# Kernel optimization log

Hardware: AMD Instinct MI355X
Metric: run time of the kernel (lower is better)

## Reference

```python
import jax, jax.numpy as jnp
import numpy as np

N_NODES = 32768
N_EDGES = 65536
IN_DIM = 3      # node feature / edge attr dim (input_size)
HID = 64        # NNConv hidden/out channels
FC1 = 128


def setup_inputs() -> dict:
    key = jax.random.key(0)
    ks = jax.random.split(key, 16)
    inp = {}
    inp["x"] = jax.random.normal(ks[0], (N_NODES, IN_DIM), dtype=jnp.float32)
    inp["edge_index"] = jax.random.randint(ks[1], (2, N_EDGES), 0, N_NODES, dtype=jnp.int64)
    inp["edge_attr"] = jax.random.normal(ks[2], (N_EDGES, IN_DIM), dtype=jnp.float32)
    s = lambda fi, fo: 1.0 / np.sqrt(fi)
    # edge MLP 1: IN_DIM -> 64 -> IN_DIM*HID
    inp["W1a"] = jax.random.normal(ks[3], (IN_DIM, 64), dtype=jnp.float32) * s(IN_DIM, 64)
    inp["b1a"] = jnp.zeros((64,), dtype=jnp.float32)
    inp["W1b"] = jax.random.normal(ks[4], (64, IN_DIM * HID), dtype=jnp.float32) * s(64, IN_DIM * HID)
    inp["b1b"] = jnp.zeros((IN_DIM * HID,), dtype=jnp.float32)
    inp["root1"] = jax.random.normal(ks[5], (IN_DIM, HID), dtype=jnp.float32) * s(IN_DIM, HID)
    inp["bias1"] = jnp.zeros((HID,), dtype=jnp.float32)
    # edge MLP 2: IN_DIM -> 64 -> HID*HID
    inp["W2a"] = jax.random.normal(ks[6], (IN_DIM, 64), dtype=jnp.float32) * s(IN_DIM, 64)
    inp["b2a"] = jnp.zeros((64,), dtype=jnp.float32)
    inp["W2b"] = jax.random.normal(ks[7], (64, HID * HID), dtype=jnp.float32) * s(64, HID * HID)
    inp["b2b"] = jnp.zeros((HID * HID,), dtype=jnp.float32)
    inp["root2"] = jax.random.normal(ks[8], (HID, HID), dtype=jnp.float32) * s(HID, HID)
    inp["bias2"] = jnp.zeros((HID,), dtype=jnp.float32)
    # fc1
    inp["Wf"] = jax.random.normal(ks[9], (HID, FC1), dtype=jnp.float32) * s(HID, FC1)
    inp["bf"] = jnp.zeros((FC1,), dtype=jnp.float32)
    return inp


def _nnconv(x, src, dst, edge_attr, Wa, ba, Wb, bb, root, bias, in_c, out_c):
    # per-edge weight matrix from edge MLP: [E, in_c, out_c]
    h = jax.nn.relu(edge_attr @ Wa + ba)
    W_e = (h @ Wb + bb).reshape(-1, in_c, out_c)
    # gather source features, transform per edge: [E, out_c]
    msg = jnp.einsum('ei,eio->eo', x[src], W_e)
    # scatter-mean into target nodes
    summed = jax.ops.segment_sum(msg, dst, num_segments=N_NODES)
    cnt = jax.ops.segment_sum(jnp.ones((msg.shape[0],), msg.dtype), dst, num_segments=N_NODES)
    agg = summed / jnp.maximum(cnt, 1.0)[:, None]
    return agg + x @ root + bias


def reference(x, edge_index, edge_attr, W1a, b1a, W1b, b1b, root1, bias1,
              W2a, b2a, W2b, b2b, root2, bias2, Wf, bf):
    src, dst = edge_index[0], edge_index[1]
    h = jax.nn.elu(_nnconv(x, src, dst, edge_attr, W1a, b1a, W1b, b1b, root1, bias1, IN_DIM, HID))
    h = jax.nn.elu(_nnconv(h, src, dst, edge_attr, W2a, b2a, W2b, b2b, root2, bias2, HID, HID))
    h = jax.nn.elu(h @ Wf + bf)
    # dropout is identity in eval mode
    return h
```

## Files before the change

### kernel.cpp

```cpp
#include <hip/hip_runtime.h>
#include <math.h>

#define NN 32768
#define NE 65536

typedef __attribute__((ext_vector_type(8))) short bf16x8;
typedef __attribute__((ext_vector_type(4))) float f32x4;

__device__ __forceinline__ float elu_f(float v) {
    return v > 0.f ? v : (expf(v) - 1.f);
}
__device__ __forceinline__ unsigned short bf16_rn(float f) {
    unsigned u = __float_as_uint(f);
    return (unsigned short)((u + 0x7FFFu + ((u >> 16) & 1u)) >> 16);
}
__device__ __forceinline__ float bf16_to_f(unsigned short h) {
    return __uint_as_float(((unsigned)h) << 16);
}

#define FMA8(Cj, aj, b0, b1) \
    Cj[0] += (aj)*(b0).x; Cj[1] += (aj)*(b0).y; Cj[2] += (aj)*(b0).z; Cj[3] += (aj)*(b0).w; \
    Cj[4] += (aj)*(b1).x; Cj[5] += (aj)*(b1).y; Cj[6] += (aj)*(b1).z; Cj[7] += (aj)*(b1).w;

__global__ void k_hist(const int* __restrict__ ei, int* __restrict__ cnt) {
    int e = blockIdx.x * 256 + threadIdx.x;
    if (e < NE) atomicAdd(&cnt[ei[NE + e]], 1);
}

__global__ __launch_bounds__(1024) void k_scan(const int* __restrict__ cnt,
                                               int* __restrict__ start,
                                               int* __restrict__ cursor) {
    __shared__ int wtot[16];
    const int t = threadIdx.x;
    const int lane = t & 63, wave = t >> 6;
    int local[32];
    const int base = t * 32;
    int s = 0;
    #pragma unroll
    for (int j = 0; j < 32; ++j) { local[j] = s; s += cnt[base + j]; }
    const int tot = s;
    int sc = tot;
    #pragma unroll
    for (int off = 1; off < 64; off <<= 1) {
        int v = __shfl_up(sc, off, 64);
        if (lane >= off) sc += v;
    }
    if (lane == 63) wtot[wave] = sc;
    __syncthreads();
    if (t == 0) {
        int run = 0;
        #pragma unroll
        for (int w = 0; w < 16; ++w) { int v = wtot[w]; wtot[w] = run; run += v; }
    }
    __syncthreads();
    const int tbase = wtot[wave] + (sc - tot);
    #pragma unroll
    for (int j = 0; j < 32; ++j) {
        int v = tbase + local[j];
        start[base + j] = v;
        cursor[base + j] = v;
    }
}

__global__ void k_fill(const int* __restrict__ ei, int* __restrict__ cursor,
                       int* __restrict__ perm) {
    int e = blockIdx.x * 256 + threadIdx.x;
    if (e < NE) {
        int d = ei[NE + e];
        int pos = atomicAdd(&cursor[d], 1);
        perm[pos] = e;
    }
}

__global__ void k_prep(const float* __restrict__ W2b, short* __restrict__ BT) {
    int idx = blockIdx.x * 256 + threadIdx.x;
    int col = idx >> 6;
    int k   = idx & 63;
    float f = W2b[(size_t)k * 4096 + col];
    unsigned short hi = bf16_rn(f);
    unsigned short lo = bf16_rn(f - bf16_to_f(hi));
    int i = col >> 6, o = col & 63;
    size_t base = (size_t)i * 9216;
    BT[base + o * 72 + k]        = (short)hi;
    BT[base + 4608 + o * 72 + k] = (short)lo;
}

__global__ __launch_bounds__(256, 2) void k1_conv1(
    const float* __restrict__ x, const int* __restrict__ ei,
    const float* __restrict__ eatt, const int* __restrict__ perm,
    const float* __restrict__ W1a, const float* __restrict__ b1a,
    const float* __restrict__ W1b, const float* __restrict__ b1b,
    float* __restrict__ msg1)
{
    __shared__ float sW1b[64 * 192];
    __shared__ float sb1b[192];
    __shared__ float sW1a[192];
    __shared__ float sb1a[64];
    __shared__ float sxs[256 * 4];
    __shared__ float sea[256 * 4];
    const int tid = threadIdx.x;
    const int e0 = blockIdx.x * 256;

    for (int u = tid; u < 64 * 192 / 4; u += 256)
        ((float4*)sW1b)[u] = ((const float4*)W1b)[u];
    if (tid < 192) { sW1a[tid] = W1a[tid]; sb1b[tid] = b1b[tid]; }
    if (tid < 64)  sb1a[tid] = b1a[tid];
    {
        int pe = perm[e0 + tid];
        int s = ei[pe];
        sxs[tid*4+0] = x[s*3+0];
        sxs[tid*4+1] = x[s*3+1];
        sxs[tid*4+2] = x[s*3+2];
        sea[tid*4+0] = eatt[pe*3+0];
        sea[tid*4+1] = eatt[pe*3+1];
        sea[tid*4+2] = eatt[pe*3+2];
    }
    __syncthreads();

    const int ty = tid >> 3;
    const int tx = tid & 7;
    const int eb = ty * 8;
    const int o0 = tx * 8;

    float xs_r[8][3], ea_r[8][3];
    #pragma unroll
    for (int j = 0; j < 8; ++j)
        #pragma unroll
        for (int i = 0; i < 3; ++i) {
            xs_r[j][i] = sxs[(eb + j) * 4 + i];
            ea_r[j][i] = sea[(eb + j) * 4 + i];
        }

    float C[8][8];
    #pragma unroll
    for (int j = 0; j < 8; ++j)
        #pragma unroll
        for (int l = 0; l < 8; ++l) C[j][l] = 0.f;

    for (int k = 0; k < 64; ++k) {
        float hh[8];
        #pragma unroll
        for (int j = 0; j < 8; ++j) {
            float h = sb1a[k] + ea_r[j][0]*sW1a[k] + ea_r[j][1]*sW1a[64+k] + ea_r[j][2]*sW1a[128+k];
            hh[j] = fmaxf(h, 0.f);
        }
        #pragma unroll
        for (int i = 0; i < 3; ++i) {
            const float4* wp = (const float4*)&sW1b[k*192 + i*64 + o0];
            float4 w0 = wp[0], w1 = wp[1];
            float a[8];
            #pragma unroll
            for (int j = 0; j < 8; ++j) a[j] = hh[j] * xs_r[j][i];
            #pragma unroll
            for (int j = 0; j < 8; ++j) { FMA8(C[j], a[j], w0, w1); }
        }
    }
    #pragma unroll
    for (int i = 0; i < 3; ++i) {
        const float4* wp = (const float4*)&sb1b[i*64 + o0];
        float4 w0 = wp[0], w1 = wp[1];
        #pragma unroll
        for (int j = 0; j < 8; ++j) {
            float a = xs_r[j][i];
            FMA8(C[j], a, w0, w1);
        }
    }
    #pragma unroll
    for (int j = 0; j < 8; ++j) {
        float* p = msg1 + (size_t)(e0 + eb + j) * 64 + o0;
        float4 v0 = { C[j][0], C[j][1], C[j][2], C[j][3] };
        float4 v1 = { C[j][4], C[j][5], C[j][6], C[j][7] };
        *(float4*)p       = v0;
        *(float4*)(p + 4) = v1;
    }
}

__global__ __launch_bounds__(256) void k2_node1(
    const float* __restrict__ msg1, const int* __restrict__ start,
    const int* __restrict__ cnt,
    const float* __restrict__ x, const float* __restrict__ root1,
    const float* __restrict__ bias1, float* __restrict__ h1)
{
    __shared__ float sR[192], sb[64];
    const int tid = threadIdx.x;
    if (tid < 192) sR[tid] = root1[tid];
    if (tid < 64)  sb[tid] = bias1[tid];
    __syncthreads();
    const int n = blockIdx.x * 64 + (tid >> 2);
    const int c = (tid & 3) * 16;
    const int st = start[n], num = cnt[n];
    float acc[16];
    #pragma unroll
    for (int l = 0; l < 16; ++l) acc[l] = 0.f;
    for (int d = 0; d < num; ++d) {
        const float* row = &msg1[(size_t)(st + d) * 64 + c];
        #pragma unroll
        for (int q = 0; q < 4; ++q) {
            float4 v = *(const float4*)(row + q * 4);
            acc[q*4+0] += v.x; acc[q*4+1] += v.y; acc[q*4+2] += v.z; acc[q*4+3] += v.w;
        }
    }
    const float inv = 1.f / fmaxf((float)num, 1.f);
    const float x0 = x[n*3+0], x1 = x[n*3+1], x2 = x[n*3+2];
    float* hp = &h1[(size_t)n * 64 + c];
    #pragma unroll
    for (int q = 0; q < 4; ++q) {
        float4 ov;
        float* o4 = (float*)&ov;
        #pragma unroll
        for (int l = 0; l < 4; ++l) {
            int o = c + q*4 + l;
            float v = acc[q*4+l] * inv + sb[o] + x0*sR[o] + x1*sR[64+o] + x2*sR[128+o];
            o4[l] = elu_f(v);
        }
        *(float4*)(hp + q*4) = ov;
    }
}

__global__ __launch_bounds__(256, 1) void k3_mfma(
    const float* __restrict__ h1, const int* __restrict__ ei,
    const float* __restrict__ eatt, const int* __restrict__ perm,
    const float* __restrict__ W2a, const float* __restrict__ b2a,
    const short* __restrict__ BT, const float* __restrict__ b2b,
    float* __restrict__ msg2)
{
    __shared__ __align__(16) float sX[17408];
    __shared__ __align__(16) short sB[2][9216];
    __shared__ float sbb[4096];
    __shared__ float sw2a[192];
    __shared__ float sb2a2[64];

    const int tid = threadIdx.x;
    const int e0  = blockIdx.x * 256;
    const int wid = tid >> 6;
    const int lane = tid & 63;
    const int l15 = lane & 15, lhi = lane >> 4;

    if (tid < 192) sw2a[tid] = W2a[tid];
    if (tid < 64)  sb2a2[tid] = b2a[tid];
    for (int u = tid; u < 1024; u += 256) ((float4*)sbb)[u] = ((const float4*)b2b)[u];
    const int pe = perm[e0 + tid];
    const int esrc = ei[pe];
    float ea0 = eatt[pe*3+0], ea1 = eatt[pe*3+1], ea2 = eatt[pe*3+2];
    __syncthreads();

    for (int k = 0; k < 64; ++k) {
        float h = sb2a2[k] + ea0*sw2a[k] + ea1*sw2a[64+k] + ea2*sw2a[128+k];
        sX[tid*68 + k] = fmaxf(h, 0.f);
    }
    __syncthreads();

    bf16x8 ah[4][2], al[4][2];
    #pragma unroll
    for (int rt = 0; rt < 4; ++rt)
        #pragma unroll
        for (int kc = 0; kc < 2; ++kc) {
            const float* p = &sX[(wid*64 + rt*16 + l15)*68 + kc*32 + lhi*8];
            bf16x8 H, L;
            #pragma unroll
            for (int j = 0; j < 8; ++j) {
                float f = p[j];
                unsigned short hh = bf16_rn(f);
                unsigned short ll = bf16_rn(f - bf16_to_f(hh));
                H[j] = (short)hh; L[j] = (short)ll;
            }
            ah[rt][kc] = H; al[rt][kc] = L;
        }
    __syncthreads();

    {
        const float* row = h1 + (size_t)esrc * 64;
        #pragma unroll
        for (int it = 0; it < 16; ++it) {
            float4 vv = *(const float4*)(row + it*4);
            sX[(it*4+0)*260 + tid] = vv.x;
            sX[(it*4+1)*260 + tid] = vv.y;
            sX[(it*4+2)*260 + tid] = vv.z;
            sX[(it*4+3)*260 + tid] = vv.w;
        }
    }
    {
        const unsigned* src = (const unsigned*)BT;
        unsigned* dst = (unsigned*)sB[0];
        #pragma unroll
        for (int j = 0; j < 18; ++j) dst[tid + 256*j] = src[tid + 256*j];
    }
    __syncthreads();

    f32x4 acc[4][4];
    #pragma unroll
    for (int rt = 0; rt < 4; ++rt)
        #pragma unroll
        for (int ot = 0; ot < 4; ++ot) { acc[rt][ot][0]=0.f; acc[rt][ot][1]=0.f; acc[rt][ot][2]=0.f; acc[rt][ot][3]=0.f; }

    int cur = 0;
    for (int i = 0; i < 64; ++i) {
        unsigned pf[18];
        if (i < 63) {
            const unsigned* src = (const unsigned*)(BT + (size_t)(i+1) * 9216);
            #pragma unroll
            for (int j = 0; j < 18; ++j) pf[j] = src[tid + 256*j];
        }
        float vv[4][4];
        #pragma unroll
        for (int rt = 0; rt < 4; ++rt) {
            f32x4 t4 = *(const f32x4*)&sX[i*260 + wid*64 + rt*16 + lhi*4];
            vv[rt][0]=t4[0]; vv[rt][1]=t4[1]; vv[rt][2]=t4[2]; vv[rt][3]=t4[3];
        }
        const short* Bh = &sB[cur][0];
        const short* Bl = &sB[cur][4608];
        #pragma unroll
        for (int ot = 0; ot < 4; ++ot) {
            const int ob = (ot*16 + l15)*72 + lhi*8;
            bf16x8 bh0 = *(const bf16x8*)&Bh[ob];
            bf16x8 bh1 = *(const bf16x8*)&Bh[ob + 32];
            bf16x8 bl0 = *(const bf16x8*)&Bl[ob];
            bf16x8 bl1 = *(const bf16x8*)&Bl[ob + 32];
            float bb = sbb[i*64 + ot*16 + l15];
            #pragma unroll
            for (int rt = 0; rt < 4; ++rt) {
                f32x4 t = {0.f, 0.f, 0.f, 0.f};
                t = __builtin_amdgcn_mfma_f32_16x16x32_bf16(ah[rt][0], bh0, t, 0, 0, 0);
                t = __builtin_amdgcn_mfma_f32_16x16x32_bf16(al[rt][0], bh0, t, 0, 0, 0);
                t = __builtin_amdgcn_mfma_f32_16x16x32_bf16(ah[rt][0], bl0, t, 0, 0, 0);
                t = __builtin_amdgcn_mfma_f32_16x16x32_bf16(ah[rt][1], bh1, t, 0, 0, 0);
                t = __builtin_amdgcn_mfma_f32_16x16x32_bf16(al[rt][1], bh1, t, 0, 0, 0);
                t = __builtin_amdgcn_mfma_f32_16x16x32_bf16(ah[rt][1], bl1, t, 0, 0, 0);
                #pragma unroll
                for (int r = 0; r < 4; ++r)
                    acc[rt][ot][r] += vv[rt][r] * (t[r] + bb);
            }
        }
        if (i < 63) {
            unsigned* dst = (unsigned*)sB[cur ^ 1];
            #pragma unroll
            for (int j = 0; j < 18; ++j) dst[tid + 256*j] = pf[j];
            cur ^= 1;
        }
        __syncthreads();
    }

    #pragma unroll
    for (int rt = 0; rt < 4; ++rt) {
        const int rowb = e0 + wid*64 + rt*16 + lhi*4;
        #pragma unroll
        for (int ot = 0; ot < 4; ++ot) {
            const int o = ot*16 + l15;
            #pragma unroll
            for (int r = 0; r < 4; ++r)
                msg2[(size_t)(rowb + r)*64 + o] = acc[rt][ot][r];
        }
    }
}

__global__ __launch_bounds__(256, 2) void k4_final(
    const float* __restrict__ msg2, const int* __restrict__ start,
    const int* __restrict__ cnt,
    const float* __restrict__ h1,
    const float* __restrict__ root2, const float* __restrict__ bias2,
    const float* __restrict__ Wf, const float* __restrict__ bf,
    float* __restrict__ out)
{
    __shared__ float sh1[32 * 65];
    __shared__ float sh2[32 * 65];
    __shared__ float sR[64 * 64];
    __shared__ float sW[64 * 128];
    __shared__ float sb2[64];
    __shared__ float sbf[128];
    __shared__ float sinv[32];
    __shared__ int   sstart[32];
    __shared__ int   scnt[32];
    const int tid = threadIdx.x;
    const int n0 = blockIdx.x * 32;

    for (int u = tid; u < 64*64/4; u += 256) ((float4*)sR)[u] = ((const float4*)root2)[u];
    for (int u = tid; u < 64*128/4; u += 256) ((float4*)sW)[u] = ((const float4*)Wf)[u];
    if (tid < 64)  sb2[tid] = bias2[tid];
    if (tid < 128) sbf[tid] = bf[tid];
    if (tid < 32) {
        int n = n0 + tid;
        int cc = cnt[n];
        sstart[tid] = start[n];
        scnt[tid] = cc;
        sinv[tid] = 1.f / fmaxf((float)cc, 1.f);
    }
    for (int u = tid; u < 32 * 16; u += 256) {
        int n = u >> 4, i4 = (u & 15) * 4;
        float4 v = *(const float4*)&h1[(size_t)(n0 + n) * 64 + i4];
        sh1[n*65+i4] = v.x; sh1[n*65+i4+1] = v.y; sh1[n*65+i4+2] = v.z; sh1[n*65+i4+3] = v.w;
    }
    __syncthreads();

    {
        const int tn = tid >> 4;
        const int o0 = (tid & 15) * 4;
        float acc[2][4];
        #pragma unroll
        for (int j = 0; j < 2; ++j) {
            int ln = tn * 2 + j;
            int st = sstart[ln], num = scnt[ln];
            float4 a = {0.f, 0.f, 0.f, 0.f};
            for (int d = 0; d < num; ++d) {
                float4 s = *(const float4*)&msg2[(size_t)(st + d) * 64 + o0];
                a.x += s.x; a.y += s.y; a.z += s.z; a.w += s.w;
            }
            float inv = sinv[ln];
            acc[j][0] = a.x*inv + sb2[o0+0];
            acc[j][1] = a.y*inv + sb2[o0+1];
            acc[j][2] = a.z*inv + sb2[o0+2];
            acc[j][3] = a.w*inv + sb2[o0+3];
        }
        #pragma unroll 8
        for (int k = 0; k < 64; ++k) {
            float4 r = *(const float4*)&sR[k*64 + o0];
            float h0 = sh1[(tn*2)*65 + k];
            float h1v = sh1[(tn*2+1)*65 + k];
            acc[0][0] += h0*r.x; acc[0][1] += h0*r.y; acc[0][2] += h0*r.z; acc[0][3] += h0*r.w;
            acc[1][0] += h1v*r.x; acc[1][1] += h1v*r.y; acc[1][2] += h1v*r.z; acc[1][3] += h1v*r.w;
        }
        #pragma unroll
        for (int j = 0; j < 2; ++j) {
            int n = tn * 2 + j;
            #pragma unroll
            for (int l = 0; l < 4; ++l) sh2[n*65 + o0 + l] = elu_f(acc[j][l]);
        }
    }
    __syncthreads();

    {
        const int tn = tid >> 4;
        const int c0 = (tid & 15) * 8;
        float acc[2][8];
        #pragma unroll
        for (int j = 0; j < 2; ++j)
            #pragma unroll
            for (int l = 0; l < 8; ++l) acc[j][l] = sbf[c0 + l];
        #pragma unroll 8
        for (int k = 0; k < 64; ++k) {
            float4 w0 = *(const float4*)&sW[k*128 + c0];
            float4 w1 = *(const float4*)&sW[k*128 + c0 + 4];
            float h0 = sh2[(tn*2)*65 + k];
            float h1v = sh2[(tn*2+1)*65 + k];
            FMA8(acc[0], h0, w0, w1);
            FMA8(acc[1], h1v, w0, w1);
        }
        #pragma unroll
        for (int j = 0; j < 2; ++j) {
            size_t n = n0 + tn * 2 + j;
            float4 oA, oB;
            oA.x = elu_f(acc[j][0]); oA.y = elu_f(acc[j][1]); oA.z = elu_f(acc[j][2]); oA.w = elu_f(acc[j][3]);
            oB.x = elu_f(acc[j][4]); oB.y = elu_f(acc[j][5]); oB.z = elu_f(acc[j][6]); oB.w = elu_f(acc[j][7]);
            *(float4*)&out[n*128 + c0]     = oA;
            *(float4*)&out[n*128 + c0 + 4] = oB;
        }
    }
}

extern "C" void kernel_launch(void* const* d_in, const int* in_sizes, int n_in,
                              void* d_out, int out_size, void* d_ws, size_t ws_size,
                              hipStream_t stream)
{
    const float* x     = (const float*)d_in[0];
    const int*   ei    = (const int*)d_in[1];
    const float* ea    = (const float*)d_in[2];
    const float* W1a   = (const float*)d_in[3];
    const float* b1a   = (const float*)d_in[4];
    const float* W1b   = (const float*)d_in[5];
    const float* b1b   = (const float*)d_in[6];
    const float* root1 = (const float*)d_in[7];
    const float* bias1 = (const float*)d_in[8];
    const float* W2a   = (const float*)d_in[9];
    const float* b2a   = (const float*)d_in[10];
    const float* W2b   = (const float*)d_in[11];
    const float* b2b   = (const float*)d_in[12];
    const float* root2 = (const float*)d_in[13];
    const float* bias2 = (const float*)d_in[14];
    const float* Wf    = (const float*)d_in[15];
    const float* bf    = (const float*)d_in[16];
    float* out = (float*)d_out;

    float* ws    = (float*)d_ws;
    float* msg1  = ws;
    float* msg2  = ws + 4194304;
    float* h1    = ws + 8388608;
    short* BT    = (short*)(ws + 10485760);
    int*   cnt_i = (int*)(ws + 10780672);
    int*   startp= (int*)(ws + 10813440);
    int*   cursor= (int*)(ws + 10846208);
    int*   perm  = (int*)(ws + 10878976);

    hipMemsetAsync(cnt_i, 0, (size_t)NN * sizeof(int), stream);

    k_prep  <<<1024,      256, 0, stream>>>(W2b, BT);
    k_hist  <<<NE/256,    256, 0, stream>>>(ei, cnt_i);
    k_scan  <<<1,        1024, 0, stream>>>(cnt_i, startp, cursor);
    k_fill  <<<NE/256,    256, 0, stream>>>(ei, cursor, perm);
    k1_conv1<<<NE/256,    256, 0, stream>>>(x, ei, ea, perm, W1a, b1a, W1b, b1b, msg1);
    k2_node1<<<NN/64,     256, 0, stream>>>(msg1, startp, cnt_i, x, root1, bias1, h1);
    k3_mfma <<<NE/256,    256, 0, stream>>>(h1, ei, ea, perm, W2a, b2a, BT, b2b, msg2);
    k4_final<<<NN/32,     256, 0, stream>>>(msg2, startp, cnt_i, h1, root2, bias2, Wf, bf, out);
}
```

Before: 291.0 us.

## Restructure edge convs: MFMA conv1, swap k3 operand roles, gather via perm

Conv1's per-edge message is now computed with split-bf16 MFMA from a pre-packed W1b. Conv2's MFMA is reorganised: the gathered source features become the A operand and the loop runs over the 64 hidden units, with the edge-MLP activation applied as a scalar. The bias is handled as a 65th step. Edges are processed in original order (128 per block, two blocks per CU) and the node-side reductions index messages through perm. Weight tiles are streamed into LDS with global_load_lds double buffering, and the prep and histogram kernels are merged into one launch. The risk is scattered perm-indexed reads in the reduction kernels and the extra MFMA iteration.

```diff
diff --git a/kernel.cpp b/kernel.cpp
--- a/kernel.cpp
+++ b/kernel.cpp
@@ -17,14 +17,49 @@
 __device__ __forceinline__ float bf16_to_f(unsigned short h) {
     return __uint_as_float(((unsigned)h) << 16);
 }
+__device__ __forceinline__ void gld16(const void* g, void* l) {
+    __builtin_amdgcn_global_load_lds(
+        (const __attribute__((address_space(1))) unsigned int*)g,
+        (__attribute__((address_space(3))) unsigned int*)l, 16, 0, 0);
+}
 
 #define FMA8(Cj, aj, b0, b1) \
     Cj[0] += (aj)*(b0).x; Cj[1] += (aj)*(b0).y; Cj[2] += (aj)*(b0).z; Cj[3] += (aj)*(b0).w; \
     Cj[4] += (aj)*(b1).x; Cj[5] += (aj)*(b1).y; Cj[6] += (aj)*(b1).z; Cj[7] += (aj)*(b1).w;
 
-__global__ void k_hist(const int* __restrict__ ei, int* __restrict__ cnt) {
-    int e = blockIdx.x * 256 + threadIdx.x;
-    if (e < NE) atomicAdd(&cnt[ei[NE + e]], 1);
+__global__ void k_prep2(const float* __restrict__ W2b, const float* __restrict__ b2b,
+                        const float* __restrict__ W1b, const int* __restrict__ ei,
+                        short* __restrict__ BT2, short* __restrict__ BT1,
+                        int* __restrict__ cnt) {
+    int g = blockIdx.x * 256 + threadIdx.x;
+    if (g < 262144) {
+        float f = W2b[g];
+        int o = g & 63, i = (g >> 6) & 63, k = g >> 12;
+        unsigned short hi = bf16_rn(f);
+        unsigned short lo = bf16_rn(f - bf16_to_f(hi));
+        BT2[(size_t)k * 9216 + o * 72 + i]        = (short)hi;
+        BT2[(size_t)k * 9216 + 4608 + o * 72 + i] = (short)lo;
+    } else if (g < 266240) {
+        int g2 = g - 262144;
+        float f = b2b[g2];
+        int o = g2 & 63, i = g2 >> 6;
+        unsigned short hi = bf16_rn(f);
+        unsigned short lo = bf16_rn(f - bf16_to_f(hi));
+        BT2[(size_t)64 * 9216 + o * 72 + i]        = (short)hi;
+        BT2[(size_t)64 * 9216 + 4608 + o * 72 + i] = (short)lo;
+    } else if (g < 278528) {
+        int g2 = g - 266240;
+        float f = W1b[g2];
+        int col = g2 % 192, k = g2 / 192;
+        int c = col >> 6, o = col & 63;
+        unsigned short hi = bf16_rn(f);
+        unsigned short lo = bf16_rn(f - bf16_to_f(hi));
+        BT1[c * 9216 + o * 72 + k]        = (short)hi;
+        BT1[c * 9216 + 4608 + o * 72 + k] = (short)lo;
+    } else {
+        int e = g - 278528;
+        atomicAdd(&cnt[ei[NE + e]], 1);
+    }
 }
 
 __global__ __launch_bounds__(1024) void k_scan(const int* __restrict__ cnt,
@@ -72,243 +107,87 @@
     }
 }
 
-__global__ void k_prep(const float* __restrict__ W2b, short* __restrict__ BT) {
-    int idx = blockIdx.x * 256 + threadIdx.x;
-    int col = idx >> 6;
-    int k   = idx & 63;
-    float f = W2b[(size_t)k * 4096 + col];
-    unsigned short hi = bf16_rn(f);
-    unsigned short lo = bf16_rn(f - bf16_to_f(hi));
-    int i = col >> 6, o = col & 63;
-    size_t base = (size_t)i * 9216;
-    BT[base + o * 72 + k]        = (short)hi;
-    BT[base + 4608 + o * 72 + k] = (short)lo;
-}
-
 __global__ __launch_bounds__(256, 2) void k1_conv1(
     const float* __restrict__ x, const int* __restrict__ ei,
-    const float* __restrict__ eatt, const int* __restrict__ perm,
+    const float* __restrict__ eatt,
     const float* __restrict__ W1a, const float* __restrict__ b1a,
-    const float* __restrict__ W1b, const float* __restrict__ b1b,
+    const short* __restrict__ BT1, const float* __restrict__ b1b,
     float* __restrict__ msg1)
 {
-    __shared__ float sW1b[64 * 192];
-    __shared__ float sb1b[192];
+    __shared__ __align__(16) short sBT1[3 * 9216];
+    __shared__ float sxs[128 * 4];
+    __shared__ float sea[128 * 4];
     __shared__ float sW1a[192];
     __shared__ float sb1a[64];
-    __shared__ float sxs[256 * 4];
-    __shared__ float sea[256 * 4];
+    __shared__ float sb1b[192];
+
     const int tid = threadIdx.x;
-    const int e0 = blockIdx.x * 256;
-
-    for (int u = tid; u < 64 * 192 / 4; u += 256)
-        ((float4*)sW1b)[u] = ((const float4*)W1b)[u];
+    const int e0  = blockIdx.x * 128;
+    const int wid = tid >> 6;
+    const int lane = tid & 63;
+    const int l15 = lane & 15, lhi = lane >> 4;
+
+    {
+        const char* src = (const char*)BT1;
+        char* dst = (char*)&sBT1[0];
+        for (int j = wid; j < 54; j += 4)
+            gld16(src + j * 1024 + lane * 16, dst + j * 1024);
+    }
     if (tid < 192) { sW1a[tid] = W1a[tid]; sb1b[tid] = b1b[tid]; }
     if (tid < 64)  sb1a[tid] = b1a[tid];
-    {
-        int pe = perm[e0 + tid];
-        int s = ei[pe];
+    if (tid < 128) {
+        int e = e0 + tid;
+        int s = ei[e];
         sxs[tid*4+0] = x[s*3+0];
         sxs[tid*4+1] = x[s*3+1];
         sxs[tid*4+2] = x[s*3+2];
-        sea[tid*4+0] = eatt[pe*3+0];
-        sea[tid*4+1] = eatt[pe*3+1];
-        sea[tid*4+2] = eatt[pe*3+2];
-    }
-    __syncthreads();
-
-    const int ty = tid >> 3;
-    const int tx = tid & 7;
-    const int eb = ty * 8;
-    const int o0 = tx * 8;
-
-    float xs_r[8][3], ea_r[8][3];
-    #pragma unroll
-    for (int j = 0; j < 8; ++j)
-        #pragma unroll
-        for (int i = 0; i < 3; ++i) {
-            xs_r[j][i] = sxs[(eb + j) * 4 + i];
-            ea_r[j][i] = sea[(eb + j) * 4 + i];
-        }
-
-    float C[8][8];
-    #pragma unroll
-    for (int j = 0; j < 8; ++j)
-        #pragma unroll
-        for (int l = 0; l < 8; ++l) C[j][l] = 0.f;
-
-    for (int k = 0; k < 64; ++k) {
-        float hh[8];
-        #pragma unroll
-        for (int j = 0; j < 8; ++j) {
-            float h = sb1a[k] + ea_r[j][0]*sW1a[k] + ea_r[j][1]*sW1a[64+k] + ea_r[j][2]*sW1a[128+k];
-            hh[j] = fmaxf(h, 0.f);
-        }
-        #pragma unroll
-        for (int i = 0; i < 3; ++i) {
-            const float4* wp = (const float4*)&sW1b[k*192 + i*64 + o0];
-            float4 w0 = wp[0], w1 = wp[1];
-            float a[8];
-            #pragma unroll
-            for (int j = 0; j < 8; ++j) a[j] = hh[j] * xs_r[j][i];
-            #pragma unroll
-            for (int j = 0; j < 8; ++j) { FMA8(C[j], a[j], w0, w1); }
-        }
-    }
-    #pragma unroll
-    for (int i = 0; i < 3; ++i) {
-        const float4* wp = (const float4*)&sb1b[i*64 + o0];
-        float4 w0 = wp[0], w1 = wp[1];
-        #pragma unroll
-        for (int j = 0; j < 8; ++j) {
-            float a = xs_r[j][i];
-            FMA8(C[j], a, w0, w1);
-        }
-    }
-    #pragma unroll
-    for (int j = 0; j < 8; ++j) {
-        float* p = msg1 + (size_t)(e0 + eb + j) * 64 + o0;
-        float4 v0 = { C[j][0], C[j][1], C[j][2], C[j][3] };
-        float4 v1 = { C[j][4], C[j][5], C[j][6], C[j][7] };
-        *(float4*)p       = v0;
-        *(float4*)(p + 4) = v1;
-    }
-}
-
-__global__ __launch_bounds__(256) void k2_node1(
-    const float* __restrict__ msg1, const int* __restrict__ start,
-    const int* __restrict__ cnt,
-    const float* __restrict__ x, const float* __restrict__ root1,
-    const float* __restrict__ bias1, float* __restrict__ h1)
-{
-    __shared__ float sR[192], sb[64];
-    const int tid = threadIdx.x;
-    if (tid < 192) sR[tid] = root1[tid];
-    if (tid < 64)  sb[tid] = bias1[tid];
-    __syncthreads();
-    const int n = blockIdx.x * 64 + (tid >> 2);
-    const int c = (tid & 3) * 16;
-    const int st = start[n], num = cnt[n];
-    float acc[16];
-    #pragma unroll
-    for (int l = 0; l < 16; ++l) acc[l] = 0.f;
-    for (int d = 0; d < num; ++d) {
-        const float* row = &msg1[(size_t)(st + d) * 64 + c];
-        #pragma unroll
-        for (int q = 0; q < 4; ++q) {
-            float4 v = *(const float4*)(row + q * 4);
-            acc[q*4+0] += v.x; acc[q*4+1] += v.y; acc[q*4+2] += v.z; acc[q*4+3] += v.w;
-        }
-    }
-    const float inv = 1.f / fmaxf((float)num, 1.f);
-    const float x0 = x[n*3+0], x1 = x[n*3+1], x2 = x[n*3+2];
-    float* hp = &h1[(size_t)n * 64 + c];
-    #pragma unroll
-    for (int q = 0; q < 4; ++q) {
-        float4 ov;
-        float* o4 = (float*)&ov;
-        #pragma unroll
-        for (int l = 0; l < 4; ++l) {
-            int o = c + q*4 + l;
-            float v = acc[q*4+l] * inv + sb[o] + x0*sR[o] + x1*sR[64+o] + x2*sR[128+o];
-            o4[l] = elu_f(v);
-        }
-        *(float4*)(hp + q*4) = ov;
-    }
-}
-
-__global__ __launch_bounds__(256, 1) void k3_mfma(
-    const float* __restrict__ h1, const int* __restrict__ ei,
-    const float* __restrict__ eatt, const int* __restrict__ perm,
-    const float* __restrict__ W2a, const float* __restrict__ b2a,
-    const short* __restrict__ BT, const float* __restrict__ b2b,
-    float* __restrict__ msg2)
-{
-    __shared__ __align__(16) float sX[17408];
-    __shared__ __align__(16) short sB[2][9216];
-    __shared__ float sbb[4096];
-    __shared__ float sw2a[192];
-    __shared__ float sb2a2[64];
-
-    const int tid = threadIdx.x;
-    const int e0  = blockIdx.x * 256;
-    const int wid = tid >> 6;
-    const int lane = tid & 63;
-    const int l15 = lane & 15, lhi = lane >> 4;
-
-    if (tid < 192) sw2a[tid] = W2a[tid];
-    if (tid < 64)  sb2a2[tid] = b2a[tid];
-    for (int u = tid; u < 1024; u += 256) ((float4*)sbb)[u] = ((const float4*)b2b)[u];
-    const int pe = perm[e0 + tid];
-    const int esrc = ei[pe];
-    float ea0 = eatt[pe*3+0], ea1 = eatt[pe*3+1], ea2 = eatt[pe*3+2];
-    __syncthreads();
-
-    for (int k = 0; k < 64; ++k) {
-        float h = sb2a2[k] + ea0*sw2a[k] + ea1*sw2a[64+k] + ea2*sw2a[128+k];
-        sX[tid*68 + k] = fmaxf(h, 0.f);
-    }
-    __syncthreads();
-
-    bf16x8 ah[4][2], al[4][2];
-    #pragma unroll
-    for (int rt = 0; rt < 4; ++rt)
+        sea[tid*4+0] = eatt[e*3+0];
+        sea[tid*4+1] = eatt[e*3+1];
+        sea[tid*4+2] = eatt[e*3+2];
+    }
+    __syncthreads();
+
+    bf16x8 ah[2][2], al[2][2];
+    #pragma unroll
+    for (int rt = 0; rt < 2; ++rt) {
+        const int arow = wid*32 + rt*16 + l15;
+        const float a0 = sea[arow*4+0], a1 = sea[arow*4+1], a2 = sea[arow*4+2];
         #pragma unroll
         for (int kc = 0; kc < 2; ++kc) {
-            const float* p = &sX[(wid*64 + rt*16 + l15)*68 + kc*32 + lhi*8];
+            const int kb = kc*32 + lhi*8;
             bf16x8 H, L;
             #pragma unroll
             for (int j = 0; j < 8; ++j) {
-                float f = p[j];
+                int k = kb + j;
+                float f = fmaxf(sb1a[k] + a0*sW1a[k] + a1*sW1a[64+k] + a2*sW1a[128+k], 0.f);
                 unsigned short hh = bf16_rn(f);
                 unsigned short ll = bf16_rn(f - bf16_to_f(hh));
                 H[j] = (short)hh; L[j] = (short)ll;
             }
             ah[rt][kc] = H; al[rt][kc] = L;
         }
-    __syncthreads();
-
-    {
-        const float* row = h1 + (size_t)esrc * 64;
-        #pragma unroll
-        for (int it = 0; it < 16; ++it) {
-            float4 vv = *(const float4*)(row + it*4);
-            sX[(it*4+0)*260 + tid] = vv.x;
-            sX[(it*4+1)*260 + tid] = vv.y;
-            sX[(it*4+2)*260 + tid] = vv.z;
-            sX[(it*4+3)*260 + tid] = vv.w;
-        }
-    }
-    {
-        const unsigned* src = (const unsigned*)BT;
-        unsigned* dst = (unsigned*)sB[0];
-        #pragma unroll
-        for (int j = 0; j < 18; ++j) dst[tid + 256*j] = src[tid + 256*j];
-    }
-    __syncthreads();
-
-    f32x4 acc[4][4];
-    #pragma unroll
-    for (int rt = 0; rt < 4; ++rt)
+    }
+    float xr[2][4][3];
+    #pragma unroll
+    for (int rt = 0; rt < 2; ++rt)
+        #pragma unroll
+        for (int r = 0; r < 4; ++r) {
+            int crow = wid*32 + rt*16 + lhi*4 + r;
+            xr[rt][r][0] = sxs[crow*4+0];
+            xr[rt][r][1] = sxs[crow*4+1];
+            xr[rt][r][2] = sxs[crow*4+2];
+        }
+
+    f32x4 acc[2][4];
+    #pragma unroll
+    for (int rt = 0; rt < 2; ++rt)
         #pragma unroll
         for (int ot = 0; ot < 4; ++ot) { acc[rt][ot][0]=0.f; acc[rt][ot][1]=0.f; acc[rt][ot][2]=0.f; acc[rt][ot][3]=0.f; }
 
-    int cur = 0;
-    for (int i = 0; i < 64; ++i) {
-        unsigned pf[18];
-        if (i < 63) {
-            const unsigned* src = (const unsigned*)(BT + (size_t)(i+1) * 9216);
-            #pragma unroll
-            for (int j = 0; j < 18; ++j) pf[j] = src[tid + 256*j];
-        }
-        float vv[4][4];
-        #pragma unroll
-        for (int rt = 0; rt < 4; ++rt) {
-            f32x4 t4 = *(const f32x4*)&sX[i*260 + wid*64 + rt*16 + lhi*4];
-            vv[rt][0]=t4[0]; vv[rt][1]=t4[1]; vv[rt][2]=t4[2]; vv[rt][3]=t4[3];
-        }
-        const short* Bh = &sB[cur][0];
-        const short* Bl = &sB[cur][4608];
+    #pragma unroll
+    for (int c = 0; c < 3; ++c) {
+        const short* Bh = &sBT1[c * 9216];
+        const short* Bl = Bh + 4608;
         #pragma unroll
         for (int ot = 0; ot < 4; ++ot) {
             const int ob = (ot*16 + l15)*72 + lhi*8;
@@ -316,9 +195,8 @@
             bf16x8 bh1 = *(const bf16x8*)&Bh[ob + 32];
             bf16x8 bl0 = *(const bf16x8*)&Bl[ob];
             bf16x8 bl1 = *(const bf16x8*)&Bl[ob + 32];
-            float bb = sbb[i*64 + ot*16 + l15];
-            #pragma unroll
-            for (int rt = 0; rt < 4; ++rt) {
+            #pragma unroll
+            for (int rt = 0; rt < 2; ++rt) {
                 f32x4 t = {0.f, 0.f, 0.f, 0.f};
                 t = __builtin_amdgcn_mfma_f32_16x16x32_bf16(ah[rt][0], bh0, t, 0, 0, 0);
                 t = __builtin_amdgcn_mfma_f32_16x16x32_bf16(al[rt][0], bh0, t, 0, 0, 0);
@@ -328,34 +206,211 @@
                 t = __builtin_amdgcn_mfma_f32_16x16x32_bf16(ah[rt][1], bl1, t, 0, 0, 0);
                 #pragma unroll
                 for (int r = 0; r < 4; ++r)
-                    acc[rt][ot][r] += vv[rt][r] * (t[r] + bb);
-            }
-        }
-        if (i < 63) {
-            unsigned* dst = (unsigned*)sB[cur ^ 1];
-            #pragma unroll
-            for (int j = 0; j < 18; ++j) dst[tid + 256*j] = pf[j];
-            cur ^= 1;
-        }
-        __syncthreads();
-    }
-
-    #pragma unroll
-    for (int rt = 0; rt < 4; ++rt) {
-        const int rowb = e0 + wid*64 + rt*16 + lhi*4;
+                    acc[rt][ot][r] += xr[rt][r][c] * t[r];
+            }
+        }
+    }
+    #pragma unroll
+    for (int rt = 0; rt < 2; ++rt) {
         #pragma unroll
         for (int ot = 0; ot < 4; ++ot) {
             const int o = ot*16 + l15;
-            #pragma unroll
-            for (int r = 0; r < 4; ++r)
-                msg2[(size_t)(rowb + r)*64 + o] = acc[rt][ot][r];
-        }
-    }
+            const float b0 = sb1b[o], b1 = sb1b[64+o], b2 = sb1b[128+o];
+            #pragma unroll
+            for (int r = 0; r < 4; ++r) {
+                float v = acc[rt][ot][r] + xr[rt][r][0]*b0 + xr[rt][r][1]*b1 + xr[rt][r][2]*b2;
+                int row = e0 + wid*32 + rt*16 + lhi*4 + r;
+                msg1[(size_t)row * 64 + o] = v;
+            }
+        }
+    }
+}
+
+__global__ __launch_bounds__(256) void k2_node1(
+    const float* __restrict__ msg1, const int* __restrict__ start,
+    const int* __restrict__ cnt, const int* __restrict__ perm,
+    const float* __restrict__ x, const float* __restrict__ root1,
+    const float* __restrict__ bias1, float* __restrict__ h1)
+{
+    __shared__ float sR[192], sb[64];
+    const int tid = threadIdx.x;
+    if (tid < 192) sR[tid] = root1[tid];
+    if (tid < 64)  sb[tid] = bias1[tid];
+    __syncthreads();
+    const int n = blockIdx.x * 64 + (tid >> 2);
+    const int c = (tid & 3) * 16;
+    const int st = start[n], num = cnt[n];
+    float acc[16];
+    #pragma unroll
+    for (int l = 0; l < 16; ++l) acc[l] = 0.f;
+    for (int d = 0; d < num; ++d) {
+        const int row = perm[st + d];
+        const float* rp = &msg1[(size_t)row * 64 + c];
+        #pragma unroll
+        for (int q = 0; q < 4; ++q) {
+            float4 v = *(const float4*)(rp + q * 4);
+            acc[q*4+0] += v.x; acc[q*4+1] += v.y; acc[q*4+2] += v.z; acc[q*4+3] += v.w;
+        }
+    }
+    const float inv = 1.f / fmaxf((float)num, 1.f);
+    const float x0 = x[n*3+0], x1 = x[n*3+1], x2 = x[n*3+2];
+    float* hp = &h1[(size_t)n * 64 + c];
+    #pragma unroll
+    for (int q = 0; q < 4; ++q) {
+        float4 ov;
+        float* o4 = (float*)&ov;
+        #pragma unroll
+        for (int l = 0; l < 4; ++l) {
+            int o = c + q*4 + l;
+            float v = acc[q*4+l] * inv + sb[o] + x0*sR[o] + x1*sR[64+o] + x2*sR[128+o];
+            o4[l] = elu_f(v);
+        }
+        *(float4*)(hp + q*4) = ov;
+    }
+}
+
+__global__ __launch_bounds__(256, 2) void k3_mfma(
+    const float* __restrict__ h1, const int* __restrict__ ei,
+    const float* __restrict__ eatt,
+    const float* __restrict__ W2a, const float* __restrict__ b2a,
+    const short* __restrict__ BT2,
+    float* __restrict__ msg2)
+{
+    __shared__ __align__(16) float sV[128 * 68];
+    __shared__ __align__(16) short sB[2][9216];
+    __shared__ float sea[128 * 4];
+    __shared__ float sW2a[192];
+    __shared__ float sb2a[64];
+
+    const int tid = threadIdx.x;
+    const int e0  = blockIdx.x * 128;
+    const int wid = tid >> 6;
+    const int lane = tid & 63;
+    const int l15 = lane & 15, lhi = lane >> 4;
+
+    {
+        const char* src = (const char*)BT2;
+        char* dst = (char*)&sB[0][0];
+        for (int j = wid; j < 18; j += 4)
+            gld16(src + j * 1024 + lane * 16, dst + j * 1024);
+    }
+    if (tid < 192) sW2a[tid] = W2a[tid];
+    if (tid < 64)  sb2a[tid] = b2a[tid];
+    if (tid < 128) {
+        int e = e0 + tid;
+        sea[tid*4+0] = eatt[e*3+0];
+        sea[tid*4+1] = eatt[e*3+1];
+        sea[tid*4+2] = eatt[e*3+2];
+    }
+    {
+        const int edge = tid >> 1, half = tid & 1;
+        const int s = ei[e0 + edge];
+        const float* row = h1 + (size_t)s * 64 + half * 32;
+        float* dst = &sV[edge * 68 + half * 32];
+        #pragma unroll
+        for (int q = 0; q < 8; ++q)
+            *(float4*)(dst + q*4) = *(const float4*)(row + q*4);
+    }
+    __syncthreads();
+
+    bf16x8 vh[2][2], vl[2][2];
+    #pragma unroll
+    for (int rt = 0; rt < 2; ++rt)
+        #pragma unroll
+        for (int kc = 0; kc < 2; ++kc) {
+            const float* p = &sV[(wid*32 + rt*16 + l15)*68 + kc*32 + lhi*8];
+            bf16x8 H, L;
+            #pragma unroll
+            for (int j = 0; j < 8; ++j) {
+                float f = p[j];
+                unsigned short hh = bf16_rn(f);
+                unsigned short ll = bf16_rn(f - bf16_to_f(hh));
+                H[j] = (short)hh; L[j] = (short)ll;
+            }
+            vh[rt][kc] = H; vl[rt][kc] = L;
+        }
+    float er[2][4][3];
+    #pragma unroll
+    for (int rt = 0; rt < 2; ++rt)
+        #pragma unroll
+        for (int r = 0; r < 4; ++r) {
+            int row = wid*32 + rt*16 + lhi*4 + r;
+            er[rt][r][0] = sea[row*4+0];
+            er[rt][r][1] = sea[row*4+1];
+            er[rt][r][2] = sea[row*4+2];
+        }
+
+    f32x4 acc[2][4];
+    #pragma unroll
+    for (int rt = 0; rt < 2; ++rt)
+        #pragma unroll
+        for (int ot = 0; ot < 4; ++ot) { acc[rt][ot][0]=0.f; acc[rt][ot][1]=0.f; acc[rt][ot][2]=0.f; acc[rt][ot][3]=0.f; }
+
+    int cur = 0;
+    for (int k = 0; k <= 64; ++k) {
+        if (k < 64) {
+            const char* src = (const char*)(BT2 + (size_t)(k + 1) * 9216);
+            char* dst = (char*)&sB[cur ^ 1][0];
+            for (int j = wid; j < 18; j += 4)
+                gld16(src + j * 1024 + lane * 16, dst + j * 1024);
+        }
+        float us[2][4];
+        if (k < 64) {
+            const float wa = sW2a[k], wb = sW2a[64+k], wc = sW2a[128+k], bb = sb2a[k];
+            #pragma unroll
+            for (int rt = 0; rt < 2; ++rt)
+                #pragma unroll
+                for (int r = 0; r < 4; ++r)
+                    us[rt][r] = fmaxf(bb + er[rt][r][0]*wa + er[rt][r][1]*wb + er[rt][r][2]*wc, 0.f);
+        } else {
+            #pragma unroll
+            for (int rt = 0; rt < 2; ++rt)
+                #pragma unroll
+                for (int r = 0; r < 4; ++r) us[rt][r] = 1.f;
+        }
+        const short* Bh = &sB[cur][0];
+        const short* Bl = &sB[cur][4608];
+        #pragma unroll
+        for (int ot = 0; ot < 4; ++ot) {
+            const int ob = (ot*16 + l15)*72 + lhi*8;
+            bf16x8 bh0 = *(const bf16x8*)&Bh[ob];
+            bf16x8 bh1 = *(const bf16x8*)&Bh[ob + 32];
+            bf16x8 bl0 = *(const bf16x8*)&Bl[ob];
+            bf16x8 bl1 = *(const bf16x8*)&Bl[ob + 32];
+            #pragma unroll
+            for (int rt = 0; rt < 2; ++rt) {
+                f32x4 t = {0.f, 0.f, 0.f, 0.f};
+                t = __builtin_amdgcn_mfma_f32_16x16x32_bf16(vh[rt][0], bh0, t, 0, 0, 0);
+                t = __builtin_amdgcn_mfma_f32_16x16x32_bf16(vl[rt][0], bh0, t, 0, 0, 0);
+                t = __builtin_amdgcn_mfma_f32_16x16x32_bf16(vh[rt][0], bl0, t, 0, 0, 0);
+                t = __builtin_amdgcn_mfma_f32_16x16x32_bf16(vh[rt][1], bh1, t, 0, 0, 0);
+                t = __builtin_amdgcn_mfma_f32_16x16x32_bf16(vl[rt][1], bh1, t, 0, 0, 0);
+                t = __builtin_amdgcn_mfma_f32_16x16x32_bf16(vh[rt][1], bl1, t, 0, 0, 0);
+                #pragma unroll
+                for (int r = 0; r < 4; ++r)
+                    acc[rt][ot][r] += us[rt][r] * t[r];
+            }
+        }
+        __syncthreads();
+        if (k < 64) cur ^= 1;
+    }
+
+    #pragma unroll
+    for (int rt = 0; rt < 2; ++rt)
+        #pragma unroll
+        for (int ot = 0; ot < 4; ++ot) {
+            const int o = ot*16 + l15;
+            #pragma unroll
+            for (int r = 0; r < 4; ++r) {
+                int row = e0 + wid*32 + rt*16 + lhi*4 + r;
+                msg2[(size_t)row * 64 + o] = acc[rt][ot][r];
+            }
+        }
 }
 
 __global__ __launch_bounds__(256, 2) void k4_final(
     const float* __restrict__ msg2, const int* __restrict__ start,
-    const int* __restrict__ cnt,
+    const int* __restrict__ cnt, const int* __restrict__ perm,
     const float* __restrict__ h1,
     const float* __restrict__ root2, const float* __restrict__ bias2,
     const float* __restrict__ Wf, const float* __restrict__ bf,
@@ -401,7 +456,8 @@
             int st = sstart[ln], num = scnt[ln];
             float4 a = {0.f, 0.f, 0.f, 0.f};
             for (int d = 0; d < num; ++d) {
-                float4 s = *(const float4*)&msg2[(size_t)(st + d) * 64 + o0];
+                int row = perm[st + d];
+                float4 s = *(const float4*)&msg2[(size_t)row * 64 + o0];
                 a.x += s.x; a.y += s.y; a.z += s.z; a.w += s.w;
             }
             float inv = sinv[ln];
@@ -483,20 +539,20 @@
     float* msg1  = ws;
     float* msg2  = ws + 4194304;
     float* h1    = ws + 8388608;
-    short* BT    = (short*)(ws + 10485760);
-    int*   cnt_i = (int*)(ws + 10780672);
-    int*   startp= (int*)(ws + 10813440);
-    int*   cursor= (int*)(ws + 10846208);
-    int*   perm  = (int*)(ws + 10878976);
+    short* BT2   = (short*)(ws + 10485760);
+    short* BT1   = (short*)(ws + 10785280);
+    int*   cnt_i = (int*)(ws + 10799104);
+    int*   startp= (int*)(ws + 10831872);
+    int*   cursor= (int*)(ws + 10864640);
+    int*   perm  = (int*)(ws + 10897408);
 
     hipMemsetAsync(cnt_i, 0, (size_t)NN * sizeof(int), stream);
 
-    k_prep  <<<1024,      256, 0, stream>>>(W2b, BT);
-    k_hist  <<<NE/256,    256, 0, stream>>>(ei, cnt_i);
+    k_prep2 <<<1344,      256, 0, stream>>>(W2b, b2b, W1b, ei, BT2, BT1, cnt_i);
     k_scan  <<<1,        1024, 0, stream>>>(cnt_i, startp, cursor);
     k_fill  <<<NE/256,    256, 0, stream>>>(ei, cursor, perm);
-    k1_conv1<<<NE/256,    256, 0, stream>>>(x, ei, ea, perm, W1a, b1a, W1b, b1b, msg1);
-    k2_node1<<<NN/64,     256, 0, stream>>>(msg1, startp, cnt_i, x, root1, bias1, h1);
-    k3_mfma <<<NE/256,    256, 0, stream>>>(h1, ei, ea, perm, W2a, b2a, BT, b2b, msg2);
-    k4_final<<<NN/32,     256, 0, stream>>>(msg2, startp, cnt_i, h1, root2, bias2, Wf, bf, out);
-}
+    k1_conv1<<<NE/128,    256, 0, stream>>>(x, ei, ea, W1a, b1a, BT1, b1b, msg1);
+    k2_node1<<<NN/64,     256, 0, stream>>>(msg1, startp, cnt_i, perm, x, root1, bias1, h1);
+    k3_mfma <<<NE/128,    256, 0, stream>>>(h1, ei, ea, W2a, b2a, BT2, msg2);
+    k4_final<<<NN/32,     256, 0, stream>>>(msg2, startp, cnt_i, perm, h1, root2, bias2, Wf, bf, out);
+}
```

Result: faster. 268.7 us (-7.7%).
